# Kernel tuning notes

Measured on AMD Instinct MI355X. Metric: run time of the kernel, lower is better.

Reference implementation:

```python
import jax, jax.numpy as jnp
import numpy as np

DIM = 512
N_HEADS = 8
HEAD_DIM = DIM // N_HEADS


def setup_inputs() -> dict:
    key = jax.random.key(0)
    ks = jax.random.split(key, 11)
    B, S = 2, 2048
    s = 1.0 / np.sqrt(DIM)
    return {
        "q": jax.random.normal(ks[0], (B, S, DIM), jnp.float32),
        "k": jax.random.normal(ks[1], (B, S, DIM), jnp.float32),
        "v": jax.random.normal(ks[2], (B, S, DIM), jnp.float32),
        "Wq": jax.random.normal(ks[3], (DIM, DIM), jnp.float32) * s,
        "bq": jnp.zeros((DIM,), jnp.float32),
        "Wk": jax.random.normal(ks[4], (DIM, DIM), jnp.float32) * s,
        "bk": jnp.zeros((DIM,), jnp.float32),
        "Wv": jax.random.normal(ks[5], (DIM, DIM), jnp.float32) * s,
        "bv": jnp.zeros((DIM,), jnp.float32),
        "Wo": jax.random.normal(ks[6], (DIM, DIM), jnp.float32) * s,
        "bo": jnp.zeros((DIM,), jnp.float32),
    }


def reference(q, k, v, Wq, bq, Wk, bk, Wv, bv, Wo, bo):
    B, S, _ = q.shape
    # projections; split into heads: [B, H, S, Dh]
    def proj(x, W, b):
        y = x @ W.T + b
        return y.reshape(B, -1, N_HEADS, HEAD_DIM).transpose(0, 2, 1, 3)

    qh = proj(q, Wq, bq)
    kh = proj(k, Wk, bk)
    vh = proj(v, Wv, bv)
    scores = jnp.einsum("bhsd,bhtd->bhst", qh, kh) / np.sqrt(HEAD_DIM)
    attn = jax.nn.softmax(scores, axis=-1)  # dropout = identity in eval
    ctx = jnp.einsum("bhst,bhtd->bhsd", attn, vh)
    ctx = ctx.transpose(0, 2, 1, 3).reshape(B, S, DIM)
    out = ctx @ Wo.T + bo
    return out, attn
```

## Files before the change

### kernel.cpp

```cpp
#include <hip/hip_runtime.h>
#include <math.h>

#define DIM 512
#define NH 8
#define HD 64
#define SS 2048
#define NB 2

typedef __bf16 bf16;
typedef __attribute__((ext_vector_type(8))) __bf16 bf16x8;
typedef __attribute__((ext_vector_type(4))) __bf16 bf16x4;
typedef __attribute__((ext_vector_type(2))) __bf16 bf16x2;
typedef __attribute__((ext_vector_type(4))) float f32x4;

__device__ inline bf16x8 cvt8(const float* s) {
  bf16x8 o;
#pragma unroll
  for (int i = 0; i < 8; ++i) o[i] = (bf16)s[i];
  return o;
}

__device__ inline void bar_lds_only() {
  asm volatile("s_waitcnt lgkmcnt(0)" ::: "memory");
  __builtin_amdgcn_s_barrier();
}

__global__ __launch_bounds__(256) void qkv_proj_kernel(
    const float* __restrict__ xq, const float* __restrict__ xk, const float* __restrict__ xv,
    const float* __restrict__ Wq, const float* __restrict__ bq,
    const float* __restrict__ Wk, const float* __restrict__ bk,
    const float* __restrict__ Wv, const float* __restrict__ bv,
    bf16* __restrict__ qh, bf16* __restrict__ kh, bf16* __restrict__ vh)
{
  const int which = blockIdx.z;
  const float* A    = (which == 0) ? xq : (which == 1) ? xk : xv;
  const float* W    = (which == 0) ? Wq : (which == 1) ? Wk : Wv;
  const float* bias = (which == 0) ? bq : (which == 1) ? bk : bv;
  bf16* out         = (which == 0) ? qh : (which == 1) ? kh : vh;
  const float oscale = (which == 0) ? 0.125f : 1.0f;

  __shared__ bf16 As[128][72];
  __shared__ bf16 Bs[64][72];

  const int m0 = blockIdx.x * 128;
  const int n0 = blockIdx.y * 64;
  const int tid = threadIdx.x;
  const int w = tid >> 6, l = tid & 63;
  const int l16 = l & 15, lg = l >> 4;
  const int wm = w >> 1, wn = w & 1;

  f32x4 acc[4][2];
#pragma unroll
  for (int mf = 0; mf < 4; ++mf)
#pragma unroll
    for (int nf = 0; nf < 2; ++nf) acc[mf][nf] = (f32x4){0.f, 0.f, 0.f, 0.f};

  for (int k0 = 0; k0 < DIM; k0 += 64) {
    __syncthreads();
    {
      const int r = tid >> 1, hf = (tid & 1) * 32;
      const float* src = &A[(size_t)(m0 + r) * DIM + k0 + hf];
      bf16* dst = &As[r][hf];
#pragma unroll
      for (int i = 0; i < 4; ++i) ((bf16x8*)dst)[i] = cvt8(src + i * 8);
    }
    if (tid < 128) {
      const int r = tid >> 1, hf = (tid & 1) * 32;
      const float* src = &W[(size_t)(n0 + r) * DIM + k0 + hf];
      bf16* dst = &Bs[r][hf];
#pragma unroll
      for (int i = 0; i < 4; ++i) ((bf16x8*)dst)[i] = cvt8(src + i * 8);
    }
    __syncthreads();

#pragma unroll
    for (int kk = 0; kk < 2; ++kk) {
      bf16x8 bfr[2];
      bfr[0] = *(const bf16x8*)&Bs[wn * 32 + l16][kk * 32 + lg * 8];
      bfr[1] = *(const bf16x8*)&Bs[wn * 32 + 16 + l16][kk * 32 + lg * 8];
#pragma unroll
      for (int mf = 0; mf < 4; ++mf) {
        const bf16x8 af = *(const bf16x8*)&As[wm * 64 + mf * 16 + l16][kk * 32 + lg * 8];
        acc[mf][0] = __builtin_amdgcn_mfma_f32_16x16x32_bf16(af, bfr[0], acc[mf][0], 0, 0, 0);
        acc[mf][1] = __builtin_amdgcn_mfma_f32_16x16x32_bf16(af, bfr[1], acc[mf][1], 0, 0, 0);
      }
    }
  }

  const int h = blockIdx.y;
#pragma unroll
  for (int mf = 0; mf < 4; ++mf) {
#pragma unroll
    for (int nf = 0; nf < 2; ++nf) {
      const int d = wn * 32 + nf * 16 + l16;
#pragma unroll
      for (int ri = 0; ri < 4; ++ri) {
        const int row = m0 + wm * 64 + mf * 16 + lg * 4 + ri;
        const int b = row >> 11, s = row & 2047;
        out[((size_t)(b * NH + h) * SS + s) * HD + d] =
            (bf16)((acc[mf][nf][ri] + bias[n0 + d]) * oscale);
      }
    }
  }
}

__global__ __launch_bounds__(512, 4) void attn_kernel(
    const bf16* __restrict__ qh, const bf16* __restrict__ kh, const bf16* __restrict__ vh,
    float* __restrict__ attn, bf16* __restrict__ ctx)
{
  __shared__ __align__(16) bf16 Ks[2][64][72];
  __shared__ __align__(16) bf16 Vt[2][64][72];
  __shared__ __align__(16) bf16 Ps[8][16][128];
  __shared__ float mlred[2][4][16];

  const int lin  = blockIdx.x;
  const int work = (lin & 7) * 64 + (lin >> 3);
  const int bh = work >> 5;
  const int q0 = (work & 31) * 64;

  const int tid = threadIdx.x;
  const int w   = tid >> 6;
  const int wq  = w >> 1;
  const int wt  = w & 1;
  const int l   = tid & 63;
  const int l16 = l & 15;
  const int lg  = l >> 4;

  const bf16* qp = qh + (size_t)bh * SS * HD;
  const bf16* kp = kh + (size_t)bh * SS * HD;
  const bf16* vp = vh + (size_t)bh * SS * HD;

  const int ks_wt = tid >> 8;
  const int ks_r  = (tid >> 2) & 63;
  const int ks_c  = (tid & 3) * 16;
  const int vs_wt = tid >> 8;
  const int vs_rc = (tid >> 3) & 31;
  const int vs_dc = tid & 7;

  const int qrow = q0 + wq * 16 + l16;
  const bf16x8 qf0 = *(const bf16x8*)&qp[(size_t)qrow * HD + lg * 8];
  const bf16x8 qf1 = *(const bf16x8*)&qp[(size_t)qrow * HD + 32 + lg * 8];

  const int tbase = wt * 1024;

  float lsum = 0.f;
  for (int tt = 0; tt < 1024; tt += 64) {
    bar_lds_only();
    {
      const bf16* src = &kp[(size_t)(ks_wt * 1024 + tt + ks_r) * HD + ks_c];
      bf16* dst = &Ks[ks_wt][ks_r][ks_c];
      ((bf16x8*)dst)[0] = ((const bf16x8*)src)[0];
      ((bf16x8*)dst)[1] = ((const bf16x8*)src)[1];
    }
    bar_lds_only();

#pragma unroll
    for (int n = 0; n < 4; ++n) {
      const bf16x8 kf0 = *(const bf16x8*)&Ks[wt][n * 16 + l16][lg * 8];
      const bf16x8 kf1 = *(const bf16x8*)&Ks[wt][n * 16 + l16][32 + lg * 8];
      f32x4 a = {0.f, 0.f, 0.f, 0.f};
      a = __builtin_amdgcn_mfma_f32_16x16x32_bf16(kf0, qf0, a, 0, 0, 0);
      a = __builtin_amdgcn_mfma_f32_16x16x32_bf16(kf1, qf1, a, 0, 0, 0);
#pragma unroll
      for (int reg = 0; reg < 4; ++reg) lsum += __expf(a[reg]);
    }
  }
  lsum += __shfl_xor(lsum, 16);
  lsum += __shfl_xor(lsum, 32);
  if (lg == 0) mlred[wt][wq][l16] = lsum;
  __syncthreads();
  const float inv_l = 1.f / (mlred[0][wq][l16] + mlred[1][wq][l16]);

  f32x4 accC[4];
#pragma unroll
  for (int dt = 0; dt < 4; ++dt) accC[dt] = (f32x4){0.f, 0.f, 0.f, 0.f};

  float* arow = attn + ((size_t)(bh * SS + q0 + wq * 16 + l16)) * SS + tbase;
  char* psbase = (char*)&Ps[w][0][0] + l16 * 256;

  for (int tt = 0; tt < 1024; tt += 64) {
    bar_lds_only();
    {
      const bf16* src = &kp[(size_t)(ks_wt * 1024 + tt + ks_r) * HD + ks_c];
      bf16* dst = &Ks[ks_wt][ks_r][ks_c];
      ((bf16x8*)dst)[0] = ((const bf16x8*)src)[0];
      ((bf16x8*)dst)[1] = ((const bf16x8*)src)[1];
    }
    {
      const bf16* vsrc = &vp[(size_t)(vs_wt * 1024 + tt + vs_rc * 2) * HD + vs_dc * 8];
      const bf16x8 v0 = *(const bf16x8*)vsrc;
      const bf16x8 v1 = *(const bf16x8*)(vsrc + HD);
      const int colbase = (((vs_rc >> 2) ^ vs_dc) << 3) | ((vs_rc & 3) << 1);
#pragma unroll
      for (int j = 0; j < 8; ++j) {
        *(bf16x2*)&Vt[vs_wt][vs_dc * 8 + j][colbase] = (bf16x2){v0[j], v1[j]};
      }
    }
    bar_lds_only();

#pragma unroll
    for (int n = 0; n < 4; ++n) {
      const bf16x8 kf0 = *(const bf16x8*)&Ks[wt][n * 16 + l16][lg * 8];
      const bf16x8 kf1 = *(const bf16x8*)&Ks[wt][n * 16 + l16][32 + lg * 8];
      f32x4 a = {0.f, 0.f, 0.f, 0.f};
      a = __builtin_amdgcn_mfma_f32_16x16x32_bf16(kf0, qf0, a, 0, 0, 0);
      a = __builtin_amdgcn_mfma_f32_16x16x32_bf16(kf1, qf1, a, 0, 0, 0);

      float4 pv;
      bf16x4 p4;
#pragma unroll
      for (int reg = 0; reg < 4; ++reg) {
        const float p = __expf(a[reg]) * inv_l;
        ((float*)&pv)[reg] = p;
        p4[reg] = (bf16)p;
      }
      *(float4*)&arow[tt + n * 16 + lg * 4] = pv;
      *(bf16x4*)(psbase + ((((n << 1) | (lg >> 1)) ^ (l16 & 7)) << 4) + ((lg & 1) << 3)) = p4;
    }

#pragma unroll
    for (int ts = 0; ts < 2; ++ts) {
      const bf16x8 pa = *(const bf16x8*)(psbase + ((((ts << 2) | lg) ^ (l16 & 7)) << 4));
#pragma unroll
      for (int dt = 0; dt < 4; ++dt) {
        const int vcol = (((ts * 4 + lg) ^ ((dt * 2 + (l16 >> 3)) & 7)) << 3);
        const bf16x8 vb = *(const bf16x8*)&Vt[wt][dt * 16 + l16][vcol];
        accC[dt] = __builtin_amdgcn_mfma_f32_16x16x32_bf16(vb, pa, accC[dt], 0, 0, 0);
      }
    }
  }

  __syncthreads();
  float* cred = (float*)&Ks[0][0][0];
  if (wt == 1) {
#pragma unroll
    for (int dt = 0; dt < 4; ++dt)
      *(f32x4*)&cred[(wq * 16 + l16) * 68 + dt * 16 + lg * 4] = accC[dt];
  }
  __syncthreads();
  if (wt == 0) {
    const int b = bh >> 3, h = bh & 7;
    bf16* crow = ctx + ((size_t)b * SS + q0 + wq * 16 + l16) * DIM + h * HD;
#pragma unroll
    for (int dt = 0; dt < 4; ++dt) {
      const f32x4 o = *(const f32x4*)&cred[(wq * 16 + l16) * 68 + dt * 16 + lg * 4];
      bf16x4 cb;
#pragma unroll
      for (int reg = 0; reg < 4; ++reg) cb[reg] = (bf16)(accC[dt][reg] + o[reg]);
      *(bf16x4*)&crow[dt * 16 + lg * 4] = cb;
    }
  }
}

__global__ __launch_bounds__(256) void out_proj_kernel(
    const bf16* __restrict__ ctx, const float* __restrict__ Wo, const float* __restrict__ bo,
    float* __restrict__ out)
{
  __shared__ bf16 As[128][72];
  __shared__ bf16 Bs[64][72];

  const int m0 = blockIdx.x * 128;
  const int n0 = blockIdx.y * 64;
  const int tid = threadIdx.x;
  const int w = tid >> 6, l = tid & 63;
  const int l16 = l & 15, lg = l >> 4;
  const int wm = w >> 1, wn = w & 1;

  f32x4 acc[4][2];
#pragma unroll
  for (int mf = 0; mf < 4; ++mf)
#pragma unroll
    for (int nf = 0; nf < 2; ++nf) acc[mf][nf] = (f32x4){0.f, 0.f, 0.f, 0.f};

  for (int k0 = 0; k0 < DIM; k0 += 64) {
    __syncthreads();
    {
      const int r = tid >> 1, hf = (tid & 1) * 32;
      const bf16* src = &ctx[(size_t)(m0 + r) * DIM + k0 + hf];
      bf16* dst = &As[r][hf];
#pragma unroll
      for (int i = 0; i < 4; ++i) ((bf16x8*)dst)[i] = ((const bf16x8*)src)[i];
    }
    if (tid < 128) {
      const int r = tid >> 1, hf = (tid & 1) * 32;
      const float* src = &Wo[(size_t)(n0 + r) * DIM + k0 + hf];
      bf16* dst = &Bs[r][hf];
#pragma unroll
      for (int i = 0; i < 4; ++i) ((bf16x8*)dst)[i] = cvt8(src + i * 8);
    }
    __syncthreads();

#pragma unroll
    for (int kk = 0; kk < 2; ++kk) {
      bf16x8 bfr[2];
      bfr[0] = *(const bf16x8*)&Bs[wn * 32 + l16][kk * 32 + lg * 8];
      bfr[1] = *(const bf16x8*)&Bs[wn * 32 + 16 + l16][kk * 32 + lg * 8];
#pragma unroll
      for (int mf = 0; mf < 4; ++mf) {
        const bf16x8 af = *(const bf16x8*)&As[wm * 64 + mf * 16 + l16][kk * 32 + lg * 8];
        acc[mf][0] = __builtin_amdgcn_mfma_f32_16x16x32_bf16(af, bfr[0], acc[mf][0], 0, 0, 0);
        acc[mf][1] = __builtin_amdgcn_mfma_f32_16x16x32_bf16(af, bfr[1], acc[mf][1], 0, 0, 0);
      }
    }
  }

#pragma unroll
  for (int mf = 0; mf < 4; ++mf) {
#pragma unroll
    for (int nf = 0; nf < 2; ++nf) {
      const int c = n0 + wn * 32 + nf * 16 + l16;
#pragma unroll
      for (int ri = 0; ri < 4; ++ri) {
        const int row = m0 + wm * 64 + mf * 16 + lg * 4 + ri;
        out[(size_t)row * DIM + c] = acc[mf][nf][ri] + bo[c];
      }
    }
  }
}

extern "C" void kernel_launch(void* const* d_in, const int* in_sizes, int n_in,
                              void* d_out, int out_size, void* d_ws, size_t ws_size,
                              hipStream_t stream) {
  const float* q  = (const float*)d_in[0];
  const float* k  = (const float*)d_in[1];
  const float* v  = (const float*)d_in[2];
  const float* Wq = (const float*)d_in[3];
  const float* bq = (const float*)d_in[4];
  const float* Wk = (const float*)d_in[5];
  const float* bk = (const float*)d_in[6];
  const float* Wv = (const float*)d_in[7];
  const float* bv = (const float*)d_in[8];
  const float* Wo = (const float*)d_in[9];
  const float* bo = (const float*)d_in[10];

  float* out0 = (float*)d_out;
  float* attn = out0 + (size_t)NB * SS * DIM;

  const size_t HSZ = (size_t)NB * NH * SS * HD;
  bf16* qh  = (bf16*)d_ws;
  bf16* kh  = qh + HSZ;
  bf16* vh  = kh + HSZ;
  bf16* ctx = vh + HSZ;

  dim3 g1(NB * SS / 128, DIM / 64, 3);
  qkv_proj_kernel<<<g1, 256, 0, stream>>>(q, k, v, Wq, bq, Wk, bk, Wv, bv, qh, kh, vh);

  dim3 g2(SS / 64 * NB * NH);
  attn_kernel<<<g2, 512, 0, stream>>>(qh, kh, vh, attn, ctx);

  dim3 g3(NB * SS / 128, DIM / 64);
  out_proj_kernel<<<g3, 256, 0, stream>>>(ctx, Wo, bo, out0);
}
```

Baseline: 142.7 us.

## Prefetch next K/V tiles into registers while computing current tile

Both attention passes now issue the global loads for the next K (and V) tile into registers before computing on the current LDS tile. After a barrier they write those registers to LDS. This is meant to hide global load latency behind the MFMA and exp work instead of stalling on loads at the start of each iteration. It costs extra registers for the staged tiles, which may lower occupancy, and it keeps two barriers per iteration.

```diff
diff --git a/kernel.cpp b/kernel.cpp
--- a/kernel.cpp
+++ b/kernel.cpp
@@ -137,6 +137,11 @@
   const int vs_rc = (tid >> 3) & 31;
   const int vs_dc = tid & 7;
 
+  const bf16* kstage = &kp[(size_t)(ks_wt * 1024 + ks_r) * HD + ks_c];
+  const bf16* vstage = &vp[(size_t)(vs_wt * 1024 + vs_rc * 2) * HD + vs_dc * 8];
+  bf16* ks_dst = &Ks[ks_wt][ks_r][ks_c];
+  const int vcolbase = (((vs_rc >> 2) ^ vs_dc) << 3) | ((vs_rc & 3) << 1);
+
   const int qrow = q0 + wq * 16 + l16;
   const bf16x8 qf0 = *(const bf16x8*)&qp[(size_t)qrow * HD + lg * 8];
   const bf16x8 qf1 = *(const bf16x8*)&qp[(size_t)qrow * HD + 32 + lg * 8];
@@ -144,13 +149,18 @@
   const int tbase = wt * 1024;
 
   float lsum = 0.f;
+  {
+    const bf16* src = kstage;
+    ((bf16x8*)ks_dst)[0] = ((const bf16x8*)src)[0];
+    ((bf16x8*)ks_dst)[1] = ((const bf16x8*)src)[1];
+  }
   for (int tt = 0; tt < 1024; tt += 64) {
-    bar_lds_only();
-    {
-      const bf16* src = &kp[(size_t)(ks_wt * 1024 + tt + ks_r) * HD + ks_c];
-      bf16* dst = &Ks[ks_wt][ks_r][ks_c];
-      ((bf16x8*)dst)[0] = ((const bf16x8*)src)[0];
-      ((bf16x8*)dst)[1] = ((const bf16x8*)src)[1];
+    bf16x8 kr0, kr1;
+    const bool has_next = (tt + 64) < 1024;
+    if (has_next) {
+      const bf16* src = kstage + (size_t)(tt + 64) * HD;
+      kr0 = ((const bf16x8*)src)[0];
+      kr1 = ((const bf16x8*)src)[1];
     }
     bar_lds_only();
 
@@ -164,6 +174,11 @@
 #pragma unroll
       for (int reg = 0; reg < 4; ++reg) lsum += __expf(a[reg]);
     }
+    bar_lds_only();
+    if (has_next) {
+      ((bf16x8*)ks_dst)[0] = kr0;
+      ((bf16x8*)ks_dst)[1] = kr1;
+    }
   }
   lsum += __shfl_xor(lsum, 16);
   lsum += __shfl_xor(lsum, 32);
@@ -178,23 +193,28 @@
   float* arow = attn + ((size_t)(bh * SS + q0 + wq * 16 + l16)) * SS + tbase;
   char* psbase = (char*)&Ps[w][0][0] + l16 * 256;
 
+  {
+    const bf16* src = kstage;
+    ((bf16x8*)ks_dst)[0] = ((const bf16x8*)src)[0];
+    ((bf16x8*)ks_dst)[1] = ((const bf16x8*)src)[1];
+    const bf16x8 v0 = *(const bf16x8*)vstage;
+    const bf16x8 v1 = *(const bf16x8*)(vstage + HD);
+#pragma unroll
+    for (int j = 0; j < 8; ++j) {
+      *(bf16x2*)&Vt[vs_wt][vs_dc * 8 + j][vcolbase] = (bf16x2){v0[j], v1[j]};
+    }
+  }
+
   for (int tt = 0; tt < 1024; tt += 64) {
-    bar_lds_only();
-    {
-      const bf16* src = &kp[(size_t)(ks_wt * 1024 + tt + ks_r) * HD + ks_c];
-      bf16* dst = &Ks[ks_wt][ks_r][ks_c];
-      ((bf16x8*)dst)[0] = ((const bf16x8*)src)[0];
-      ((bf16x8*)dst)[1] = ((const bf16x8*)src)[1];
-    }
-    {
-      const bf16* vsrc = &vp[(size_t)(vs_wt * 1024 + tt + vs_rc * 2) * HD + vs_dc * 8];
-      const bf16x8 v0 = *(const bf16x8*)vsrc;
-      const bf16x8 v1 = *(const bf16x8*)(vsrc + HD);
-      const int colbase = (((vs_rc >> 2) ^ vs_dc) << 3) | ((vs_rc & 3) << 1);
-#pragma unroll
-      for (int j = 0; j < 8; ++j) {
-        *(bf16x2*)&Vt[vs_wt][vs_dc * 8 + j][colbase] = (bf16x2){v0[j], v1[j]};
-      }
+    bf16x8 kr0, kr1, vr0, vr1;
+    const bool has_next = (tt + 64) < 1024;
+    if (has_next) {
+      const bf16* ksrc = kstage + (size_t)(tt + 64) * HD;
+      kr0 = ((const bf16x8*)ksrc)[0];
+      kr1 = ((const bf16x8*)ksrc)[1];
+      const bf16* vsrc = vstage + (size_t)(tt + 64) * HD;
+      vr0 = *(const bf16x8*)vsrc;
+      vr1 = *(const bf16x8*)(vsrc + HD);
     }
     bar_lds_only();
 
@@ -226,6 +246,15 @@
         const int vcol = (((ts * 4 + lg) ^ ((dt * 2 + (l16 >> 3)) & 7)) << 3);
         const bf16x8 vb = *(const bf16x8*)&Vt[wt][dt * 16 + l16][vcol];
         accC[dt] = __builtin_amdgcn_mfma_f32_16x16x32_bf16(vb, pa, accC[dt], 0, 0, 0);
+      }
+    }
+    bar_lds_only();
+    if (has_next) {
+      ((bf16x8*)ks_dst)[0] = kr0;
+      ((bf16x8*)ks_dst)[1] = kr1;
+#pragma unroll
+      for (int j = 0; j < 8; ++j) {
+        *(bf16x2*)&Vt[vs_wt][vs_dc * 8 + j][vcolbase] = (bf16x2){vr0[j], vr1[j]};
       }
     }
   }
```

Result: no change. 140.2 us (-1.8%).
